# Kernel tuning notes

Measured on AMD Instinct MI355X. Metric: run time of the kernel, lower is better.

The kernel has to match this reference:

```python
import jax, jax.numpy as jnp
import numpy as np

NUM_GENES = 8192
NUM_SETS = 256
BATCH = 32
ALPHA = 0.25


def setup_inputs() -> dict:
    key = jax.random.key(0)
    k1, k2, k3 = jax.random.split(key, 3)
    R = jax.random.uniform(k1, (BATCH, NUM_GENES), dtype=jnp.float32)
    # S is a per-sample permutation of gene indices (sort order)
    S = jnp.argsort(jax.random.uniform(k2, (BATCH, NUM_GENES)), axis=1).astype(jnp.int32)
    W = jax.random.normal(k3, (NUM_SETS, NUM_GENES), dtype=jnp.float32)  # set_membership
    return {"R": R, "S": S, "W": W}


def _set_indicators(W):
    ind = jax.nn.sigmoid(W)  # (M, G)
    avg = ind.mean(axis=1, keepdims=True)
    return jnp.where(ind < avg * 0.3, ind * 0.01, ind)


def reference(R, S, W):
    batch, num_genes = R.shape
    ind = _set_indicators(W)                                   # (M, G)
    # gather indicators per sample's sort order: (B, M, G)
    sorted_ind = jnp.transpose(ind[:, S], (1, 0, 2))
    R_sorted = jnp.take_along_axis(R, S, axis=1)               # (B, G)
    clamped = jnp.clip(R_sorted[:, None, :] * sorted_ind, 1e-8, 1e4)
    wpos = clamped ** ALPHA                                    # (B, M, G)
    sum_pos = jnp.sum(wpos, axis=2, keepdims=True)
    cdf_pos = jnp.where(sum_pos > 1e-8,
                        jnp.cumsum(wpos, axis=2) / (sum_pos + 1e-10),
                        jnp.zeros_like(wpos))
    neg = (sorted_ind < 0.1).astype(R.dtype)                   # (B, M, G)
    sum_neg = jnp.sum(neg, axis=2, keepdims=True)
    cdf_neg = jnp.where(sum_neg > 1e-8,
                        jnp.cumsum(neg, axis=2) / (sum_neg + 1e-10),
                        jnp.zeros_like(neg))
    diff = (cdf_pos - cdf_neg) / num_genes
    return jnp.sum(diff, axis=2)                               # (B, M)
```

## Files before the change

### kernel.cpp

```cpp
#include <hip/hip_runtime.h>
#include <math.h>

constexpr int NG  = 8192;
constexpr int NM  = 256;
constexpr int NB  = 32;
constexpr int KR  = 256;
constexpr int NKB = NG / KR;


using bf16x8 = __attribute__((ext_vector_type(8))) short;
using s16x4  = __attribute__((ext_vector_type(4))) short;
using f32x4  = __attribute__((ext_vector_type(4))) float;

__device__ __forceinline__ float sigmoidf(float x) {
  return __builtin_amdgcn_rcpf(1.0f + __builtin_amdgcn_exp2f(x * -1.442695041f));
}
__device__ __forceinline__ float qrtf(float x) {
  return __builtin_amdgcn_sqrtf(__builtin_amdgcn_sqrtf(x));
}
__device__ __forceinline__ short bfr(float f) {
  unsigned x = __float_as_uint(f);
  return (short)((x + 0x7fffu + ((x >> 16) & 1u)) >> 16);
}

__global__ __launch_bounds__(256) void k_prep(const int* __restrict__ S,
                                              const float* __restrict__ W,
                                              const float* __restrict__ R,
                                              unsigned short* __restrict__ pA,
                                              unsigned short* __restrict__ pB,
                                              float* __restrict__ sumN) {
  const int tid = threadIdx.x;

  if (blockIdx.x < NM) {
    __shared__ float red[4];
    const int m = blockIdx.x;
    const float4* w4 = reinterpret_cast<const float4*>(W + (size_t)m * NG);
    float4 sg[8];
    float s = 0.f;
    #pragma unroll
    for (int q = 0; q < 8; ++q) {
      float4 v = w4[q * 256 + tid];
      sg[q] = make_float4(sigmoidf(v.x), sigmoidf(v.y), sigmoidf(v.z), sigmoidf(v.w));
      s += sg[q].x + sg[q].y + sg[q].z + sg[q].w;
    }
    #pragma unroll
    for (int off = 32; off > 0; off >>= 1) s += __shfl_xor(s, off, 64);
    if ((tid & 63) == 0) red[tid >> 6] = s;
    __syncthreads();
    const float tm = (red[0] + red[1] + red[2] + red[3]) * (0.3f / (float)NG);
    float sn = 0.f;
    s16x4* dst = reinterpret_cast<s16x4*>(pA + (size_t)m * NG);
    #pragma unroll
    for (int q = 0; q < 8; ++q) {
      float vv[4] = {sg[q].x, sg[q].y, sg[q].z, sg[q].w};
      s16x4 po;
      #pragma unroll
      for (int j = 0; j < 4; ++j) {
        float v = vv[j];
        v = (v < tm) ? v * 0.01f : v;
        const bool ng = v < 0.1f;
        po[j] = (short)(bfr(qrtf(v)) | (ng ? (short)0x8000 : (short)0));
        sn += ng ? 1.f : 0.f;
      }
      dst[q * 256 + tid] = po;
    }
    #pragma unroll
    for (int off = 32; off > 0; off >>= 1) sn += __shfl_xor(sn, off, 64);
    if ((tid & 63) == 0) red[tid >> 6] = sn;
    __syncthreads();
    if (tid == 0) sumN[m] = red[0] + red[1] + red[2] + red[3];
  } else {
    __shared__ float row[NG];
    const int b = blockIdx.x - NM;
    const int4* s4 = reinterpret_cast<const int4*>(S + (size_t)b * NG);
    #pragma unroll
    for (int q = 0; q < 8; ++q) {
      const int i = q * 256 + tid;
      const int4 g4 = s4[i];
      const int k = i * 4;
      row[g4.x] = (float)(NG - k);
      row[g4.y] = (float)(NG - (k + 1));
      row[g4.z] = (float)(NG - (k + 2));
      row[g4.w] = (float)(NG - (k + 3));
    }
    __syncthreads();
    const float4* r4 = reinterpret_cast<const float4*>(R + (size_t)b * NG);
    const float4* c4 = reinterpret_cast<const float4*>(row);
    s16x4* dra = reinterpret_cast<s16x4*>(pB + 0 * (size_t)NB * NG + (size_t)b * NG);
    s16x4* drc = reinterpret_cast<s16x4*>(pB + 1 * (size_t)NB * NG + (size_t)b * NG);
    s16x4* dcf = reinterpret_cast<s16x4*>(pB + 2 * (size_t)NB * NG + (size_t)b * NG);
    #pragma unroll
    for (int q = 0; q < 8; ++q) {
      const float4 r = r4[q * 256 + tid];
      const float4 c = c4[q * 256 + tid];
      const float ra[4] = {qrtf(r.x), qrtf(r.y), qrtf(r.z), qrtf(r.w)};
      const float cc[4] = {c.x, c.y, c.z, c.w};
      s16x4 pra, prc, pcf;
      #pragma unroll
      for (int j = 0; j < 4; ++j) {
        pra[j] = bfr(ra[j]);
        prc[j] = bfr(ra[j] * cc[j]);
        pcf[j] = bfr(cc[j]);
      }
      dra[q * 256 + tid] = pra;
      drc[q * 256 + tid] = prc;
      dcf[q * 256 + tid] = pcf;
    }
  }
}

__global__ __launch_bounds__(256) void k_mm(const unsigned short* __restrict__ pA,
                                            const unsigned short* __restrict__ pB,
                                            float* __restrict__ part) {
  const int tid  = threadIdx.x;
  const int kb   = blockIdx.x;
  const int mt   = blockIdx.y;
  const int wv   = tid >> 6;
  const int mw   = wv >> 1, bw = wv & 1;
  const int lane = tid & 63;
  const int lr   = lane & 15, lk = lane >> 4;

  const int m = mt * 32 + mw * 16 + lr;
  const int b = bw * 16 + lr;

  const unsigned short* Arow = pA + (size_t)m * NG;
  const unsigned short* Bra  = pB + 0 * (size_t)NB * NG + (size_t)b * NG;
  const unsigned short* Brc  = pB + 1 * (size_t)NB * NG + (size_t)b * NG;
  const unsigned short* Bcf  = pB + 2 * (size_t)NB * NG + (size_t)b * NG;

  f32x4 accA = {0.f, 0.f, 0.f, 0.f};
  f32x4 accB = {0.f, 0.f, 0.f, 0.f};
  f32x4 accC = {0.f, 0.f, 0.f, 0.f};

  #pragma unroll
  for (int c = 0; c < KR / 32; ++c) {
    const int g = kb * KR + c * 32 + lk * 8;

    const int4 aw = *reinterpret_cast<const int4*>(Arow + g);
    int4 iaw, nfw;
    iaw.x = aw.x & 0x7FFF7FFF;  iaw.y = aw.y & 0x7FFF7FFF;
    iaw.z = aw.z & 0x7FFF7FFF;  iaw.w = aw.w & 0x7FFF7FFF;
    nfw.x = (int)(((unsigned)(aw.x & 0x80008000) >> 15) * 0x3F80u);
    nfw.y = (int)(((unsigned)(aw.y & 0x80008000) >> 15) * 0x3F80u);
    nfw.z = (int)(((unsigned)(aw.z & 0x80008000) >> 15) * 0x3F80u);
    nfw.w = (int)(((unsigned)(aw.w & 0x80008000) >> 15) * 0x3F80u);
    const bf16x8 fia = __builtin_bit_cast(bf16x8, iaw);
    const bf16x8 fnf = __builtin_bit_cast(bf16x8, nfw);

    const bf16x8 fra = *reinterpret_cast<const bf16x8*>(Bra + g);
    const bf16x8 frc = *reinterpret_cast<const bf16x8*>(Brc + g);
    const bf16x8 fcf = *reinterpret_cast<const bf16x8*>(Bcf + g);

    accA = __builtin_amdgcn_mfma_f32_16x16x32_bf16(fia, fra, accA, 0, 0, 0);
    accB = __builtin_amdgcn_mfma_f32_16x16x32_bf16(fia, frc, accB, 0, 0, 0);
    accC = __builtin_amdgcn_mfma_f32_16x16x32_bf16(fnf, fcf, accC, 0, 0, 0);
  }

  const int md = mt * 32 + mw * 16 + 4 * lk;
  const int bd = bw * 16 + lr;
  #pragma unroll
  for (int i = 0; i < 4; ++i) {
    part[((size_t)(kb * 3 + 0) * NM + md + i) * NB + bd] = accA[i];
    part[((size_t)(kb * 3 + 1) * NM + md + i) * NB + bd] = accB[i];
    part[((size_t)(kb * 3 + 2) * NM + md + i) * NB + bd] = accC[i];
  }
}

__global__ __launch_bounds__(256) void k_final(const float* __restrict__ part,
                                               const float* __restrict__ sumN,
                                               float* __restrict__ out) {
  __shared__ float rA[256], rB[256], rC[256];
  const int tid = threadIdx.x;
  const int m   = blockIdx.x;
  const int b   = tid & 31;
  const int kg  = tid >> 5;

  float sA = 0.f, sB = 0.f, sC = 0.f;
  #pragma unroll
  for (int t = 0; t < NKB / 8; ++t) {
    const int kb = kg * (NKB / 8) + t;
    const float* p = part + ((size_t)(kb * 3) * NM + m) * NB + b;
    sA += p[0];
    sB += p[(size_t)NM * NB];
    sC += p[2 * (size_t)NM * NB];
  }
  rA[tid] = sA; rB[tid] = sB; rC[tid] = sC;
  __syncthreads();
  if (tid < 128) { rA[tid] += rA[tid + 128]; rB[tid] += rB[tid + 128]; rC[tid] += rC[tid + 128]; }
  __syncthreads();
  if (tid < 64)  { rA[tid] += rA[tid + 64];  rB[tid] += rB[tid + 64];  rC[tid] += rC[tid + 64]; }
  __syncthreads();
  if (tid < 32) {
    const float a  = rA[tid] + rA[tid + 32];
    const float bb = rB[tid] + rB[tid + 32];
    const float c  = rC[tid] + rC[tid + 32];
    const float sN = sumN[m];
    out[(size_t)tid * NM + m] = (bb / (a + 1e-10f) - c / (sN + 1e-10f)) * (1.0f / (float)NG);
  }
}

extern "C" void kernel_launch(void* const* d_in, const int* in_sizes, int n_in,
                              void* d_out, int out_size, void* d_ws, size_t ws_size,
                              hipStream_t stream) {
  const float* R = (const float*)d_in[0];
  const int*   S = (const int*)d_in[1];
  const float* W = (const float*)d_in[2];
  float* out = (float*)d_out;

  char* ws = (char*)d_ws;
  unsigned short* pA = (unsigned short*)ws;
  unsigned short* pB = pA + (size_t)NM * NG;
  float* part = (float*)(ws + (size_t)NM * NG * 2 + (size_t)3 * NB * NG * 2);
  float* sumN = part + (size_t)NKB * 3 * NM * NB;

  k_prep <<<dim3(NM + NB), dim3(256), 0, stream>>>(S, W, R, pA, pB, sumN);
  k_mm   <<<dim3(NKB, NM / 32), dim3(256), 0, stream>>>(pA, pB, part);
  k_final<<<dim3(NM), dim3(256), 0, stream>>>(part, sumN, out);
}
```

Before: 20.41 us.

## Fuse final reduction into matmul kernel via last-block atomic counter

Removes the separate k_final launch. Each k_mm block fences its partials and bumps a per-m-tile atomic counter, and the last block to arrive for that tile reduces all K-slice partials and writes the output. The counters are zeroed in k_prep. This saves one kernel launch and its gap, but the final reduction now runs serially in only 8 blocks, each thread looping over 32 K slices.

```diff
diff --git a/kernel.cpp b/kernel.cpp
--- a/kernel.cpp
+++ b/kernel.cpp
@@ -28,12 +28,14 @@
                                               const float* __restrict__ R,
                                               unsigned short* __restrict__ pA,
                                               unsigned short* __restrict__ pB,
-                                              float* __restrict__ sumN) {
+                                              float* __restrict__ sumN,
+                                              unsigned* __restrict__ cnt) {
   const int tid = threadIdx.x;
 
   if (blockIdx.x < NM) {
     __shared__ float red[4];
     const int m = blockIdx.x;
+    if (m == 0 && tid < 8) cnt[tid] = 0;
     const float4* w4 = reinterpret_cast<const float4*>(W + (size_t)m * NG);
     float4 sg[8];
     float s = 0.f;
@@ -111,7 +113,10 @@
 
 __global__ __launch_bounds__(256) void k_mm(const unsigned short* __restrict__ pA,
                                             const unsigned short* __restrict__ pB,
-                                            float* __restrict__ part) {
+                                            float* __restrict__ part,
+                                            const float* __restrict__ sumN,
+                                            unsigned* __restrict__ cnt,
+                                            float* __restrict__ out) {
   const int tid  = threadIdx.x;
   const int kb   = blockIdx.x;
   const int mt   = blockIdx.y;
@@ -164,38 +169,39 @@
     part[((size_t)(kb * 3 + 1) * NM + md + i) * NB + bd] = accB[i];
     part[((size_t)(kb * 3 + 2) * NM + md + i) * NB + bd] = accC[i];
   }
-}
-
-__global__ __launch_bounds__(256) void k_final(const float* __restrict__ part,
-                                               const float* __restrict__ sumN,
-                                               float* __restrict__ out) {
-  __shared__ float rA[256], rB[256], rC[256];
-  const int tid = threadIdx.x;
-  const int m   = blockIdx.x;
-  const int b   = tid & 31;
-  const int kg  = tid >> 5;
-
-  float sA = 0.f, sB = 0.f, sC = 0.f;
+
+  __threadfence();
+  __shared__ int is_last;
+  if (tid == 0) {
+    const unsigned t = atomicAdd(&cnt[mt], 1u);
+    is_last = (t == (unsigned)(NKB - 1)) ? 1 : 0;
+  }
+  __syncthreads();
+  if (!is_last) return;
+  __threadfence();
+
+  const int q  = tid >> 5;
+  const int fb = tid & 31;
+  float sA[4] = {0.f, 0.f, 0.f, 0.f};
+  float sB[4] = {0.f, 0.f, 0.f, 0.f};
+  float sC[4] = {0.f, 0.f, 0.f, 0.f};
+  #pragma unroll 4
+  for (int k2 = 0; k2 < NKB; ++k2) {
+    #pragma unroll
+    for (int i = 0; i < 4; ++i) {
+      const int mm = mt * 32 + q * 4 + i;
+      const float* p = part + ((size_t)(k2 * 3) * NM + mm) * NB + fb;
+      sA[i] += p[0];
+      sB[i] += p[(size_t)NM * NB];
+      sC[i] += p[2 * (size_t)NM * NB];
+    }
+  }
   #pragma unroll
-  for (int t = 0; t < NKB / 8; ++t) {
-    const int kb = kg * (NKB / 8) + t;
-    const float* p = part + ((size_t)(kb * 3) * NM + m) * NB + b;
-    sA += p[0];
-    sB += p[(size_t)NM * NB];
-    sC += p[2 * (size_t)NM * NB];
-  }
-  rA[tid] = sA; rB[tid] = sB; rC[tid] = sC;
-  __syncthreads();
-  if (tid < 128) { rA[tid] += rA[tid + 128]; rB[tid] += rB[tid + 128]; rC[tid] += rC[tid + 128]; }
-  __syncthreads();
-  if (tid < 64)  { rA[tid] += rA[tid + 64];  rB[tid] += rB[tid + 64];  rC[tid] += rC[tid + 64]; }
-  __syncthreads();
-  if (tid < 32) {
-    const float a  = rA[tid] + rA[tid + 32];
-    const float bb = rB[tid] + rB[tid + 32];
-    const float c  = rC[tid] + rC[tid + 32];
-    const float sN = sumN[m];
-    out[(size_t)tid * NM + m] = (bb / (a + 1e-10f) - c / (sN + 1e-10f)) * (1.0f / (float)NG);
+  for (int i = 0; i < 4; ++i) {
+    const int mm = mt * 32 + q * 4 + i;
+    const float sN = sumN[mm];
+    out[(size_t)fb * NM + mm] =
+        (sB[i] / (sA[i] + 1e-10f) - sC[i] / (sN + 1e-10f)) * (1.0f / (float)NG);
   }
 }
 
@@ -212,8 +218,8 @@
   unsigned short* pB = pA + (size_t)NM * NG;
   float* part = (float*)(ws + (size_t)NM * NG * 2 + (size_t)3 * NB * NG * 2);
   float* sumN = part + (size_t)NKB * 3 * NM * NB;
-
-  k_prep <<<dim3(NM + NB), dim3(256), 0, stream>>>(S, W, R, pA, pB, sumN);
-  k_mm   <<<dim3(NKB, NM / 32), dim3(256), 0, stream>>>(pA, pB, part);
-  k_final<<<dim3(NM), dim3(256), 0, stream>>>(part, sumN, out);
-}
+  unsigned* cnt = (unsigned*)(sumN + NM);
+
+  k_prep <<<dim3(NM + NB), dim3(256), 0, stream>>>(S, W, R, pA, pB, sumN, cnt);
+  k_mm   <<<dim3(NKB, NM / 32), dim3(256), 0, stream>>>(pA, pB, part, sumN, cnt, out);
+}
```

Measured after the change: 62.40 us. +205.7%, slower.
